# Kernel tuning notes

Hardware: AMD Instinct MI355X
Metric: run time of the kernel (lower is better)

The kernel has to match this reference:

```python
import jax, jax.numpy as jnp
import numpy as np

B, C, H, W = 8, 512, 32, 32
NUM_HEADS = 8
HEAD_DIM = C // NUM_HEADS
SCALE = 1.0 / float(np.sqrt(HEAD_DIM))


def setup_inputs() -> dict:
    key = jax.random.key(0)
    ks = jax.random.split(key, 6)
    x = jax.random.normal(ks[0], (B, C, H, W), dtype=jnp.float32)
    attn_mask = jax.random.randint(ks[1], (B, H, W), 0, 2).astype(jnp.bool_)
    # 1x1 conv weights are equivalent to channel matmuls: (out_ch, in_ch)
    w_std = 1.0 / float(np.sqrt(C))
    qkv_w = jax.random.uniform(ks[2], (3 * C, C), jnp.float32, -w_std, w_std)
    qkv_b = jax.random.uniform(ks[3], (3 * C,), jnp.float32, -w_std, w_std)
    proj_w = jax.random.uniform(ks[4], (C, C), jnp.float32, -w_std, w_std)
    proj_b = jax.random.uniform(ks[5], (C,), jnp.float32, -w_std, w_std)
    return {"x": x, "attn_mask": attn_mask, "qkv_w": qkv_w, "qkv_b": qkv_b,
            "proj_w": proj_w, "proj_b": proj_b}


def reference(x, attn_mask, qkv_w, qkv_b, proj_w, proj_b):
    b, c, h, w = x.shape
    S = h * w
    neg = jnp.finfo(x.dtype).min
    # qkv 1x1 conv: (B,3C,H,W)
    qkv = jnp.einsum('oc,bchw->bohw', qkv_w, x) + qkv_b[None, :, None, None]
    q, k, v = jnp.split(qkv, 3, axis=1)

    def split_heads(z):
        # (B, C, H, W) -> (B, heads, head_dim, S)
        return z.reshape(b, NUM_HEADS, HEAD_DIM, S)

    q, k, v = split_heads(q), split_heads(k), split_heads(v)
    # scores[s,t] = sum_d q[d,s] * k[d,t]
    scores = jnp.einsum('bhds,bhdt->bhst', q, k) * SCALE
    idx = jnp.arange(S)
    causal = (idx[None, :] > idx[:, None])[None, None]  # (1,1,S,S), True above diag
    scores = jnp.where(causal, neg, scores)
    kpm = attn_mask.reshape(b, 1, 1, S)  # key padding mask, True = mask out
    scores = jnp.where(kpm, neg, scores)
    attn = jax.nn.softmax(scores, axis=-1)
    # ctx[d,s] = sum_t v[d,t] * attn[s,t]
    ctx = jnp.einsum('bhdt,bhst->bhds', v, attn)
    ctx = ctx.reshape(b, c, h, w)
    out = jnp.einsum('oc,bchw->bohw', proj_w, ctx) + proj_b[None, :, None, None]
    return out
```

## Files before the change

### kernel.cpp

```cpp
#include <hip/hip_runtime.h>
#include <cfloat>
#include <math.h>

#define SB 1024
#define CC 512
#define NB 8
#define NH 8
#define HD 64

typedef short short8 __attribute__((ext_vector_type(8)));
typedef short s16x4 __attribute__((ext_vector_type(4)));
typedef float f32x4 __attribute__((ext_vector_type(4)));

__device__ __forceinline__ short f2bs(float f) {
    union { float f; unsigned u; } x; x.f = f;
    unsigned r = x.u + 0x7fffu + ((x.u >> 16) & 1u);
    return (short)(r >> 16);
}

__device__ __forceinline__ float bs2f(short s) {
    union { unsigned u; float f; } x;
    x.u = ((unsigned)(unsigned short)s) << 16;
    return x.f;
}

__device__ __forceinline__ void gload16(const void* g, void* l) {
    __builtin_amdgcn_global_load_lds(
        (const __attribute__((address_space(1))) unsigned int*)g,
        (__attribute__((address_space(3))) unsigned int*)l, 16, 0, 0);
}

__device__ __forceinline__ int sidx(int row, int colb) {
    return row * 64 + ((colb ^ ((row & 7) << 4)) >> 1);
}

__global__ __launch_bounds__(256)
void cvt_weights(const float* __restrict__ w1, const float* __restrict__ w2,
                 short* __restrict__ o1, short* __restrict__ o2)
{
    const int i4 = blockIdx.x * 256 + threadIdx.x;
    const int N1 = 1536 * 512 / 4;
    if (i4 < N1) {
        float4 v = *(const float4*)&w1[(size_t)i4 * 4];
        s16x4 p; p[0] = f2bs(v.x); p[1] = f2bs(v.y); p[2] = f2bs(v.z); p[3] = f2bs(v.w);
        *(s16x4*)&o1[(size_t)i4 * 4] = p;
    } else {
        const int j = i4 - N1;
        float4 v = *(const float4*)&w2[(size_t)j * 4];
        s16x4 p; p[0] = f2bs(v.x); p[1] = f2bs(v.y); p[2] = f2bs(v.z); p[3] = f2bs(v.w);
        *(s16x4*)&o2[(size_t)j * 4] = p;
    }
}

__global__ __launch_bounds__(256)
void transpose_x(const float* __restrict__ x, short* __restrict__ xT)
{
    const int bs = blockIdx.x, bc = blockIdx.y, b = blockIdx.z;
    const int tid = threadIdx.x;
    __shared__ short T[64][72];
    {
        const int cl = tid >> 4;
        const int s4 = (tid & 15) * 4;
        #pragma unroll
        for (int r = 0; r < 4; ++r) {
            const int c = cl + 16 * r;
            float4 v = *(const float4*)&x[((size_t)b * CC + bc * 64 + c) * SB + bs * 64 + s4];
            T[s4 + 0][c] = f2bs(v.x); T[s4 + 1][c] = f2bs(v.y);
            T[s4 + 2][c] = f2bs(v.z); T[s4 + 3][c] = f2bs(v.w);
        }
    }
    __syncthreads();
    {
        const int sl = tid >> 2;
        const int c16 = (tid & 3) * 16;
        short8 v0 = *(const short8*)&T[sl][c16];
        short8 v1 = *(const short8*)&T[sl][c16 + 8];
        short* dst = &xT[((size_t)b * SB + bs * 64 + sl) * CC + bc * 64 + c16];
        *(short8*)&dst[0] = v0;
        *(short8*)&dst[8] = v1;
    }
}

__global__ __launch_bounds__(256)
void vmean_kernel(const short* __restrict__ vN, const int* __restrict__ mask,
                  float* __restrict__ vmean, float* __restrict__ maskf)
{
    const int gi = blockIdx.x * 256 + threadIdx.x;
    if (gi < NB * SB) maskf[gi] = (mask[gi] != 0) ? -FLT_MAX : 0.f;

    const int row = blockIdx.x * 4 + (threadIdx.x >> 6);
    const int lane = threadIdx.x & 63;
    const short* p = vN + (size_t)row * SB + lane * 16;
    short8 a = *(const short8*)&p[0];
    short8 b8 = *(const short8*)&p[8];
    float s = 0.f;
    #pragma unroll
    for (int j = 0; j < 8; ++j) s += bs2f(a[j]) + bs2f(b8[j]);
    #pragma unroll
    for (int o = 1; o < 64; o <<= 1) s += __shfl_xor(s, o, 64);
    if (lane == 0) vmean[row] = s * (1.f / 1024.f);
}

template<int MODE>
__global__ __launch_bounds__(256)
void gemm_bf16(const short* __restrict__ A, const float* __restrict__ bias,
               const short* __restrict__ BT,
               short* __restrict__ qTo, short* __restrict__ kTo,
               short* __restrict__ vo, float* __restrict__ fo)
{
    const int stile = blockIdx.x * 128;
    const int bo    = blockIdx.y;
    const int b     = blockIdx.z;
    const int tid   = threadIdx.x;
    const int wave = tid >> 6, lane = tid & 63, lg = lane >> 4, ln = lane & 15;
    const int wm = wave >> 1, wn = wave & 1;

    __shared__ short Al[128 * 64];
    __shared__ short Bl[128 * 64];

    f32x4 acc[4][4];
    #pragma unroll
    for (int mt = 0; mt < 4; ++mt)
        #pragma unroll
        for (int nt = 0; nt < 4; ++nt) acc[mt][nt] = (f32x4){0.f, 0.f, 0.f, 0.f};

    const char* Ab = (const char*)(A + (size_t)bo * 128 * 512);
    const char* Bb = (const char*)(BT + ((size_t)b * SB + stile) * 512);

    for (int kc = 0; kc < 512; kc += 64) {
        __syncthreads();
        #pragma unroll
        for (int sw = 0; sw < 4; ++sw) {
            const int lin = tid * 16 + sw * 4096;
            const int row = lin >> 7;
            const int scol = (lin & 127) ^ ((row & 7) << 4);
            gload16(Ab + ((size_t)row * 512 + kc) * 2 + scol,
                    (char*)Al + (wave << 10) + (sw << 12));
            gload16(Bb + ((size_t)row * 512 + kc) * 2 + scol,
                    (char*)Bl + (wave << 10) + (sw << 12));
        }
        __syncthreads();
        #pragma unroll
        for (int kk = 0; kk < 2; ++kk) {
            const int colb = kk * 64 + lg * 16;
            short8 a[4], bb[4];
            #pragma unroll
            for (int mt = 0; mt < 4; ++mt)
                a[mt] = *(const short8*)&Al[sidx(wm * 64 + mt * 16 + ln, colb)];
            #pragma unroll
            for (int nt = 0; nt < 4; ++nt)
                bb[nt] = *(const short8*)&Bl[sidx(wn * 64 + nt * 16 + ln, colb)];
            #pragma unroll
            for (int mt = 0; mt < 4; ++mt)
                #pragma unroll
                for (int nt = 0; nt < 4; ++nt)
                    acc[mt][nt] = __builtin_amdgcn_mfma_f32_16x16x32_bf16(
                        a[mt], bb[nt], acc[mt][nt], 0, 0, 0);
        }
    }

    const int s_base = stile + wn * 64;
    if (MODE == 0) {
        if (bo < 8) {
            short* dst = (bo < 4) ? qTo : kTo;
            const int h = (bo & 3) * 2 + wm;
            const float sc = (bo < 4) ? 0.18033688011112042f : 1.0f;
            #pragma unroll
            for (int mt = 0; mt < 4; ++mt) {
                const int d0 = mt * 16 + 4 * lg;
                const int o0 = bo * 128 + wm * 64 + d0;
                const float b0 = bias[o0], b1 = bias[o0 + 1],
                            b2 = bias[o0 + 2], b3 = bias[o0 + 3];
                #pragma unroll
                for (int nt = 0; nt < 4; ++nt) {
                    const int s = s_base + nt * 16 + ln;
                    s16x4 pk;
                    pk[0] = f2bs((acc[mt][nt][0] + b0) * sc);
                    pk[1] = f2bs((acc[mt][nt][1] + b1) * sc);
                    pk[2] = f2bs((acc[mt][nt][2] + b2) * sc);
                    pk[3] = f2bs((acc[mt][nt][3] + b3) * sc);
                    *(s16x4*)&dst[(((size_t)b * NH + h) * SB + s) * HD + d0] = pk;
                }
            }
        } else {
            #pragma unroll
            for (int mt = 0; mt < 4; ++mt) {
                const int cv0 = (bo - 8) * 128 + wm * 64 + mt * 16 + 4 * lg;
                #pragma unroll
                for (int r = 0; r < 4; ++r) {
                    const float bv = bias[1024 + cv0 + r];
                    #pragma unroll
                    for (int nt = 0; nt < 4; ++nt) {
                        const int s = s_base + nt * 16 + ln;
                        vo[((size_t)b * CC + cv0 + r) * SB + s] = f2bs(acc[mt][nt][r] + bv);
                    }
                }
            }
        }
    } else {
        #pragma unroll
        for (int mt = 0; mt < 4; ++mt) {
            #pragma unroll
            for (int r = 0; r < 4; ++r) {
                const int o = bo * 128 + wm * 64 + mt * 16 + 4 * lg + r;
                const float bv = bias[o];
                #pragma unroll
                for (int nt = 0; nt < 4; ++nt) {
                    const int s = s_base + nt * 16 + ln;
                    fo[((size_t)b * CC + o) * SB + s] = acc[mt][nt][r] + bv;
                }
            }
        }
    }
}

__global__ __launch_bounds__(256, 4)
void attn_mfma(const short* __restrict__ qT, const short* __restrict__ kT,
               const short* __restrict__ vN, const float* __restrict__ maskf,
               const float* __restrict__ vmean, short* __restrict__ ctxT)
{
    const int L  = blockIdx.x;
    const int qb = 15 - (L >> 6);
    const int bh = L & 63;
    const int b  = bh >> 3, h = bh & 7;
    const int tid = threadIdx.x;
    const int wave = tid >> 6;
    const int lane = tid & 63;
    const int lg = lane >> 4;
    const int ln = lane & 15;

    __shared__ short Ks[2][64 * 64];
    __shared__ short Vs[2][64 * 64];
    __shared__ float mskL[2][64];
    __shared__ short Ps[4][16][72];

    const char*  kbh = (const char*)(kT + (((size_t)b * NH + h) * SB) * HD);
    const char*  vbh = (const char*)(vN + ((size_t)b * CC + h * HD) * SB);
    const float* mb  = maskf + (size_t)b * SB;

    short8 qa0, qa1;
    {
        const short* qrow = qT + (((size_t)b * NH + h) * SB + qb * 64 + wave * 16 + ln) * HD;
        qa0 = *(const short8*)&qrow[8 * lg];
        qa1 = *(const short8*)&qrow[32 + 8 * lg];
    }

    float m_ = -FLT_MAX, l_ = 0.f;
    f32x4 acc[4];
    #pragma unroll
    for (int nt = 0; nt < 4; ++nt) acc[nt] = (f32x4){0.f, 0.f, 0.f, 0.f};

    auto stage = [&](int tb, int bi) {
        #pragma unroll
        for (int sw = 0; sw < 2; ++sw) {
            const int lin = tid * 16 + sw * 4096;
            const int row = lin >> 7;
            const int scol = (lin & 127) ^ ((row & 7) << 4);
            gload16(kbh + (size_t)tb * 128 + row * 128 + scol,
                    (char*)&Ks[bi][0] + (wave << 10) + (sw << 12));
            gload16(vbh + (size_t)row * (SB * 2) + tb * 2 + scol,
                    (char*)&Vs[bi][0] + (wave << 10) + (sw << 12));
        }
        if (tid < 64) mskL[bi][tid] = mb[tb + tid];
    };

    int cur = 0;
    stage(0, 0);
    __syncthreads();

    for (int t = 0; t <= qb; ++t) {
        if (t < qb) stage((t + 1) * 64, cur ^ 1);

        f32x4 sc[4];
        #pragma unroll
        for (int nt = 0; nt < 4; ++nt) {
            short8 kb0 = *(const short8*)&Ks[cur][sidx(ln + 16 * nt, lg * 16)];
            short8 kb1 = *(const short8*)&Ks[cur][sidx(ln + 16 * nt, 64 + lg * 16)];
            f32x4 z = (f32x4){0.f, 0.f, 0.f, 0.f};
            z = __builtin_amdgcn_mfma_f32_16x16x32_bf16(kb0, qa0, z, 0, 0, 0);
            z = __builtin_amdgcn_mfma_f32_16x16x32_bf16(kb1, qa1, z, 0, 0, 0);
            sc[nt] = z;
        }

        #pragma unroll
        for (int nt = 0; nt < 4; ++nt) {
            const float4 mf = *(const float4*)&mskL[cur][16 * nt + 4 * lg];
            sc[nt][0] += mf.x; sc[nt][1] += mf.y;
            sc[nt][2] += mf.z; sc[nt][3] += mf.w;
        }
        if (t == qb) {
            const int so = wave * 16 + ln;
            #pragma unroll
            for (int nt = 0; nt < 4; ++nt)
                #pragma unroll
                for (int r = 0; r < 4; ++r)
                    if (16 * nt + 4 * lg + r > so) sc[nt][r] = -FLT_MAX;
        }

        float mx = sc[0][0];
        #pragma unroll
        for (int nt = 0; nt < 4; ++nt)
            #pragma unroll
            for (int r = 0; r < 4; ++r)
                if (nt | r) mx = fmaxf(mx, sc[nt][r]);
        mx = fmaxf(mx, __shfl_xor(mx, 16, 64));
        mx = fmaxf(mx, __shfl_xor(mx, 32, 64));

        if (!__all(mx <= m_ + 11.5f)) {
            const float mnew = fmaxf(m_, mx);
            const float fq = exp2f(m_ - mnew);
            l_ *= fq;
            #pragma unroll
            for (int nt = 0; nt < 4; ++nt)
                #pragma unroll
                for (int r = 0; r < 4; ++r) acc[nt][r] *= fq;
            m_ = mnew;
        }

        float rs = 0.f;
        #pragma unroll
        for (int nt = 0; nt < 4; ++nt) {
            s16x4 pk;
            #pragma unroll
            for (int r = 0; r < 4; ++r) {
                const float p = exp2f(sc[nt][r] - m_);
                rs += p;
                pk[r] = f2bs(p);
            }
            *(s16x4*)&Ps[wave][ln][16 * nt + 4 * lg] = pk;
        }
        rs += __shfl_xor(rs, 16, 64);
        rs += __shfl_xor(rs, 32, 64);
        l_ += rs;

        const short8 pa0 = *(const short8*)&Ps[wave][ln][8 * lg];
        const short8 pa1 = *(const short8*)&Ps[wave][ln][32 + 8 * lg];
        #pragma unroll
        for (int nt = 0; nt < 4; ++nt) {
            short8 va0 = *(const short8*)&Vs[cur][sidx(16 * nt + ln, lg * 16)];
            short8 va1 = *(const short8*)&Vs[cur][sidx(16 * nt + ln, 64 + lg * 16)];
            acc[nt] = __builtin_amdgcn_mfma_f32_16x16x32_bf16(va0, pa0, acc[nt], 0, 0, 0);
            acc[nt] = __builtin_amdgcn_mfma_f32_16x16x32_bf16(va1, pa1, acc[nt], 0, 0, 0);
        }

        if (t < qb) {
            __syncthreads();
            cur ^= 1;
        }
    }

    const float rl = 1.f / l_;
    const bool dead = (m_ == -FLT_MAX);
    const float* vmb = vmean + (size_t)b * CC + h * HD;
    const int s = qb * 64 + wave * 16 + ln;
    short* crow = ctxT + ((size_t)b * SB + s) * CC + h * HD;
    #pragma unroll
    for (int nt = 0; nt < 4; ++nt) {
        const int d0 = 16 * nt + 4 * lg;
        const float4 vm4 = *(const float4*)&vmb[d0];
        s16x4 pk;
        pk[0] = f2bs(dead ? vm4.x : acc[nt][0] * rl);
        pk[1] = f2bs(dead ? vm4.y : acc[nt][1] * rl);
        pk[2] = f2bs(dead ? vm4.z : acc[nt][2] * rl);
        pk[3] = f2bs(dead ? vm4.w : acc[nt][3] * rl);
        *(s16x4*)&crow[d0] = pk;
    }
}

extern "C" void kernel_launch(void* const* d_in, const int* in_sizes, int n_in,
                              void* d_out, int out_size, void* d_ws, size_t ws_size,
                              hipStream_t stream) {
    const float* x      = (const float*)d_in[0];
    const int*   amask  = (const int*)d_in[1];
    const float* qkv_w  = (const float*)d_in[2];
    const float* qkv_b  = (const float*)d_in[3];
    const float* proj_w = (const float*)d_in[4];
    const float* proj_b = (const float*)d_in[5];
    float* out = (float*)d_out;

    short* xT    = (short*)d_ws;
    short* w1b   = xT  + (size_t)NB * SB * CC;
    short* w2b   = w1b + (size_t)1536 * 512;
    short* qT    = w2b + (size_t)512 * 512;
    short* kT    = qT  + (size_t)NB * NH * SB * HD;
    short* vN    = kT  + (size_t)NB * NH * SB * HD;
    short* ctxT  = vN  + (size_t)NB * CC * SB;
    float* vmean = (float*)(ctxT + (size_t)NB * SB * CC);
    float* maskf = vmean + (size_t)NB * CC;

    cvt_weights<<<1024, 256, 0, stream>>>(qkv_w, proj_w, w1b, w2b);
    transpose_x<<<dim3(SB / 64, CC / 64, NB), 256, 0, stream>>>(x, xT);
    gemm_bf16<0><<<dim3(8, 12, NB), 256, 0, stream>>>(
        w1b, qkv_b, xT, qT, kT, vN, nullptr);
    vmean_kernel<<<NB * CC / 4, 256, 0, stream>>>(vN, amask, vmean, maskf);
    attn_mfma<<<dim3(1024, 1, 1), 256, 0, stream>>>(qT, kT, vN, maskf, vmean, ctxT);
    gemm_bf16<1><<<dim3(8, 4, NB), 256, 0, stream>>>(
        w2b, proj_b, ctxT, nullptr, nullptr, nullptr, out);
}
```

Baseline: 85.14 us.

## Merge prep kernels, fuse V-mean into QKV GEMM, pair query blocks in attention

The weight conversion, x transpose, mask conversion and vmean zeroing now run as one prep launch. The V row means are accumulated with atomics in the QKV GEMM epilogue, which removes the separate vmean kernel. The attention kernel now uses 512-thread blocks that each handle two query blocks (2p and 2p+1) and share the K/V tile loads between them. The two halves do unequal work, so waves of the lower query block sit idle on the last tile, and the atomics add contention and make the sums nondeterministic.

```diff
diff --git a/kernel.cpp b/kernel.cpp
--- a/kernel.cpp
+++ b/kernel.cpp
@@ -18,12 +18,6 @@
     return (short)(r >> 16);
 }
 
-__device__ __forceinline__ float bs2f(short s) {
-    union { unsigned u; float f; } x;
-    x.u = ((unsigned)(unsigned short)s) << 16;
-    return x.f;
-}
-
 __device__ __forceinline__ void gload16(const void* g, void* l) {
     __builtin_amdgcn_global_load_lds(
         (const __attribute__((address_space(1))) unsigned int*)g,
@@ -35,70 +29,59 @@
 }
 
 __global__ __launch_bounds__(256)
-void cvt_weights(const float* __restrict__ w1, const float* __restrict__ w2,
-                 short* __restrict__ o1, short* __restrict__ o2)
+void prep(const float* __restrict__ w1, const float* __restrict__ w2,
+          short* __restrict__ o1, short* __restrict__ o2,
+          const float* __restrict__ x, short* __restrict__ xT,
+          const int* __restrict__ mask, float* __restrict__ maskf,
+          float* __restrict__ vmean)
 {
-    const int i4 = blockIdx.x * 256 + threadIdx.x;
-    const int N1 = 1536 * 512 / 4;
-    if (i4 < N1) {
-        float4 v = *(const float4*)&w1[(size_t)i4 * 4];
-        s16x4 p; p[0] = f2bs(v.x); p[1] = f2bs(v.y); p[2] = f2bs(v.z); p[3] = f2bs(v.w);
-        *(s16x4*)&o1[(size_t)i4 * 4] = p;
+    const int B = blockIdx.x;
+    const int tid = threadIdx.x;
+    if (B < 1024) {
+        const int i4 = B * 256 + tid;
+        const int N1 = 1536 * 512 / 4;
+        if (i4 < N1) {
+            float4 v = *(const float4*)&w1[(size_t)i4 * 4];
+            s16x4 p; p[0] = f2bs(v.x); p[1] = f2bs(v.y); p[2] = f2bs(v.z); p[3] = f2bs(v.w);
+            *(s16x4*)&o1[(size_t)i4 * 4] = p;
+        } else {
+            const int j = i4 - N1;
+            float4 v = *(const float4*)&w2[(size_t)j * 4];
+            s16x4 p; p[0] = f2bs(v.x); p[1] = f2bs(v.y); p[2] = f2bs(v.z); p[3] = f2bs(v.w);
+            *(s16x4*)&o2[(size_t)j * 4] = p;
+        }
+    } else if (B < 2048) {
+        const int idx = B - 1024;
+        const int bs = idx & 15, bc = (idx >> 4) & 7, b = idx >> 7;
+        __shared__ short T[64][72];
+        {
+            const int cl = tid >> 4;
+            const int s4 = (tid & 15) * 4;
+            #pragma unroll
+            for (int r = 0; r < 4; ++r) {
+                const int c = cl + 16 * r;
+                float4 v = *(const float4*)&x[((size_t)b * CC + bc * 64 + c) * SB + bs * 64 + s4];
+                T[s4 + 0][c] = f2bs(v.x); T[s4 + 1][c] = f2bs(v.y);
+                T[s4 + 2][c] = f2bs(v.z); T[s4 + 3][c] = f2bs(v.w);
+            }
+        }
+        __syncthreads();
+        {
+            const int sl = tid >> 2;
+            const int c16 = (tid & 3) * 16;
+            short8 v0 = *(const short8*)&T[sl][c16];
+            short8 v1 = *(const short8*)&T[sl][c16 + 8];
+            short* dst = &xT[((size_t)b * SB + bs * 64 + sl) * CC + bc * 64 + c16];
+            *(short8*)&dst[0] = v0;
+            *(short8*)&dst[8] = v1;
+        }
+    } else if (B < 2080) {
+        const int gi = (B - 2048) * 256 + tid;
+        if (gi < NB * SB) maskf[gi] = (mask[gi] != 0) ? -FLT_MAX : 0.f;
     } else {
-        const int j = i4 - N1;
-        float4 v = *(const float4*)&w2[(size_t)j * 4];
-        s16x4 p; p[0] = f2bs(v.x); p[1] = f2bs(v.y); p[2] = f2bs(v.z); p[3] = f2bs(v.w);
-        *(s16x4*)&o2[(size_t)j * 4] = p;
-    }
-}
-
-__global__ __launch_bounds__(256)
-void transpose_x(const float* __restrict__ x, short* __restrict__ xT)
-{
-    const int bs = blockIdx.x, bc = blockIdx.y, b = blockIdx.z;
-    const int tid = threadIdx.x;
-    __shared__ short T[64][72];
-    {
-        const int cl = tid >> 4;
-        const int s4 = (tid & 15) * 4;
-        #pragma unroll
-        for (int r = 0; r < 4; ++r) {
-            const int c = cl + 16 * r;
-            float4 v = *(const float4*)&x[((size_t)b * CC + bc * 64 + c) * SB + bs * 64 + s4];
-            T[s4 + 0][c] = f2bs(v.x); T[s4 + 1][c] = f2bs(v.y);
-            T[s4 + 2][c] = f2bs(v.z); T[s4 + 3][c] = f2bs(v.w);
-        }
-    }
-    __syncthreads();
-    {
-        const int sl = tid >> 2;
-        const int c16 = (tid & 3) * 16;
-        short8 v0 = *(const short8*)&T[sl][c16];
-        short8 v1 = *(const short8*)&T[sl][c16 + 8];
-        short* dst = &xT[((size_t)b * SB + bs * 64 + sl) * CC + bc * 64 + c16];
-        *(short8*)&dst[0] = v0;
-        *(short8*)&dst[8] = v1;
-    }
-}
-
-__global__ __launch_bounds__(256)
-void vmean_kernel(const short* __restrict__ vN, const int* __restrict__ mask,
-                  float* __restrict__ vmean, float* __restrict__ maskf)
-{
-    const int gi = blockIdx.x * 256 + threadIdx.x;
-    if (gi < NB * SB) maskf[gi] = (mask[gi] != 0) ? -FLT_MAX : 0.f;
-
-    const int row = blockIdx.x * 4 + (threadIdx.x >> 6);
-    const int lane = threadIdx.x & 63;
-    const short* p = vN + (size_t)row * SB + lane * 16;
-    short8 a = *(const short8*)&p[0];
-    short8 b8 = *(const short8*)&p[8];
-    float s = 0.f;
-    #pragma unroll
-    for (int j = 0; j < 8; ++j) s += bs2f(a[j]) + bs2f(b8[j]);
-    #pragma unroll
-    for (int o = 1; o < 64; o <<= 1) s += __shfl_xor(s, o, 64);
-    if (lane == 0) vmean[row] = s * (1.f / 1024.f);
+        const int i = (B - 2080) * 256 + tid;
+        if (i < NB * CC) vmean[i] = 0.f;
+    }
 }
 
 template<int MODE>
@@ -106,7 +89,8 @@
 void gemm_bf16(const short* __restrict__ A, const float* __restrict__ bias,
                const short* __restrict__ BT,
                short* __restrict__ qTo, short* __restrict__ kTo,
-               short* __restrict__ vo, float* __restrict__ fo)
+               short* __restrict__ vo, float* __restrict__ fo,
+               float* __restrict__ vmean)
 {
     const int stile = blockIdx.x * 128;
     const int bo    = blockIdx.y;
@@ -189,11 +173,19 @@
                 #pragma unroll
                 for (int r = 0; r < 4; ++r) {
                     const float bv = bias[1024 + cv0 + r];
+                    float part = 0.f;
                     #pragma unroll
                     for (int nt = 0; nt < 4; ++nt) {
                         const int s = s_base + nt * 16 + ln;
-                        vo[((size_t)b * CC + cv0 + r) * SB + s] = f2bs(acc[mt][nt][r] + bv);
+                        const float val = acc[mt][nt][r] + bv;
+                        part += val;
+                        vo[((size_t)b * CC + cv0 + r) * SB + s] = f2bs(val);
                     }
+                    #pragma unroll
+                    for (int o = 1; o < 16; o <<= 1)
+                        part += __shfl_xor(part, o, 64);
+                    if (ln == 0)
+                        atomicAdd(&vmean[(size_t)b * CC + cv0 + r], part);
                 }
             }
         }
@@ -214,13 +206,13 @@
     }
 }
 
-__global__ __launch_bounds__(256, 4)
+__global__ __launch_bounds__(512, 4)
 void attn_mfma(const short* __restrict__ qT, const short* __restrict__ kT,
                const short* __restrict__ vN, const float* __restrict__ maskf,
                const float* __restrict__ vmean, short* __restrict__ ctxT)
 {
     const int L  = blockIdx.x;
-    const int qb = 15 - (L >> 6);
+    const int p  = 7 - (L >> 6);
     const int bh = L & 63;
     const int b  = bh >> 3, h = bh & 7;
     const int tid = threadIdx.x;
@@ -229,10 +221,14 @@
     const int lg = lane >> 4;
     const int ln = lane & 15;
 
+    const int qbm  = 2 * p + (wave >> 2);
+    const int wsub = wave & 3;
+    const int tend = 2 * p + 1;
+
     __shared__ short Ks[2][64 * 64];
     __shared__ short Vs[2][64 * 64];
     __shared__ float mskL[2][64];
-    __shared__ short Ps[4][16][72];
+    __shared__ short Ps[8][16][72];
 
     const char*  kbh = (const char*)(kT + (((size_t)b * NH + h) * SB) * HD);
     const char*  vbh = (const char*)(vN + ((size_t)b * CC + h * HD) * SB);
@@ -240,7 +236,7 @@
 
     short8 qa0, qa1;
     {
-        const short* qrow = qT + (((size_t)b * NH + h) * SB + qb * 64 + wave * 16 + ln) * HD;
+        const short* qrow = qT + (((size_t)b * NH + h) * SB + qbm * 64 + wsub * 16 + ln) * HD;
         qa0 = *(const short8*)&qrow[8 * lg];
         qa1 = *(const short8*)&qrow[32 + 8 * lg];
     }
@@ -251,16 +247,13 @@
     for (int nt = 0; nt < 4; ++nt) acc[nt] = (f32x4){0.f, 0.f, 0.f, 0.f};
 
     auto stage = [&](int tb, int bi) {
-        #pragma unroll
-        for (int sw = 0; sw < 2; ++sw) {
-            const int lin = tid * 16 + sw * 4096;
-            const int row = lin >> 7;
-            const int scol = (lin & 127) ^ ((row & 7) << 4);
-            gload16(kbh + (size_t)tb * 128 + row * 128 + scol,
-                    (char*)&Ks[bi][0] + (wave << 10) + (sw << 12));
-            gload16(vbh + (size_t)row * (SB * 2) + tb * 2 + scol,
-                    (char*)&Vs[bi][0] + (wave << 10) + (sw << 12));
-        }
+        const int lin = tid * 16;
+        const int row = lin >> 7;
+        const int scol = (lin & 127) ^ ((row & 7) << 4);
+        gload16(kbh + (size_t)tb * 128 + row * 128 + scol,
+                (char*)&Ks[bi][0] + (wave << 10));
+        gload16(vbh + (size_t)row * (SB * 2) + tb * 2 + scol,
+                (char*)&Vs[bi][0] + (wave << 10));
         if (tid < 64) mskL[bi][tid] = mb[tb + tid];
     };
 
@@ -268,82 +261,85 @@
     stage(0, 0);
     __syncthreads();
 
-    for (int t = 0; t <= qb; ++t) {
-        if (t < qb) stage((t + 1) * 64, cur ^ 1);
-
-        f32x4 sc[4];
-        #pragma unroll
-        for (int nt = 0; nt < 4; ++nt) {
-            short8 kb0 = *(const short8*)&Ks[cur][sidx(ln + 16 * nt, lg * 16)];
-            short8 kb1 = *(const short8*)&Ks[cur][sidx(ln + 16 * nt, 64 + lg * 16)];
-            f32x4 z = (f32x4){0.f, 0.f, 0.f, 0.f};
-            z = __builtin_amdgcn_mfma_f32_16x16x32_bf16(kb0, qa0, z, 0, 0, 0);
-            z = __builtin_amdgcn_mfma_f32_16x16x32_bf16(kb1, qa1, z, 0, 0, 0);
-            sc[nt] = z;
-        }
-
-        #pragma unroll
-        for (int nt = 0; nt < 4; ++nt) {
-            const float4 mf = *(const float4*)&mskL[cur][16 * nt + 4 * lg];
-            sc[nt][0] += mf.x; sc[nt][1] += mf.y;
-            sc[nt][2] += mf.z; sc[nt][3] += mf.w;
-        }
-        if (t == qb) {
-            const int so = wave * 16 + ln;
+    for (int t = 0; t <= tend; ++t) {
+        if (t < tend) stage((t + 1) * 64, cur ^ 1);
+        const bool mine = (t <= qbm);
+
+        if (mine) {
+            f32x4 sc[4];
+            #pragma unroll
+            for (int nt = 0; nt < 4; ++nt) {
+                short8 kb0 = *(const short8*)&Ks[cur][sidx(ln + 16 * nt, lg * 16)];
+                short8 kb1 = *(const short8*)&Ks[cur][sidx(ln + 16 * nt, 64 + lg * 16)];
+                f32x4 z = (f32x4){0.f, 0.f, 0.f, 0.f};
+                z = __builtin_amdgcn_mfma_f32_16x16x32_bf16(kb0, qa0, z, 0, 0, 0);
+                z = __builtin_amdgcn_mfma_f32_16x16x32_bf16(kb1, qa1, z, 0, 0, 0);
+                sc[nt] = z;
+            }
+
+            #pragma unroll
+            for (int nt = 0; nt < 4; ++nt) {
+                const float4 mf = *(const float4*)&mskL[cur][16 * nt + 4 * lg];
+                sc[nt][0] += mf.x; sc[nt][1] += mf.y;
+                sc[nt][2] += mf.z; sc[nt][3] += mf.w;
+            }
+            if (t == qbm) {
+                const int so = wsub * 16 + ln;
+                #pragma unroll
+                for (int nt = 0; nt < 4; ++nt)
+                    #pragma unroll
+                    for (int r = 0; r < 4; ++r)
+                        if (16 * nt + 4 * lg + r > so) sc[nt][r] = -FLT_MAX;
+            }
+
+            float mx = sc[0][0];
             #pragma unroll
             for (int nt = 0; nt < 4; ++nt)
                 #pragma unroll
                 for (int r = 0; r < 4; ++r)
-                    if (16 * nt + 4 * lg + r > so) sc[nt][r] = -FLT_MAX;
-        }
-
-        float mx = sc[0][0];
-        #pragma unroll
-        for (int nt = 0; nt < 4; ++nt)
-            #pragma unroll
-            for (int r = 0; r < 4; ++r)
-                if (nt | r) mx = fmaxf(mx, sc[nt][r]);
-        mx = fmaxf(mx, __shfl_xor(mx, 16, 64));
-        mx = fmaxf(mx, __shfl_xor(mx, 32, 64));
-
-        if (!__all(mx <= m_ + 11.5f)) {
-            const float mnew = fmaxf(m_, mx);
-            const float fq = exp2f(m_ - mnew);
-            l_ *= fq;
-            #pragma unroll
-            for (int nt = 0; nt < 4; ++nt)
-                #pragma unroll
-                for (int r = 0; r < 4; ++r) acc[nt][r] *= fq;
-            m_ = mnew;
-        }
-
-        float rs = 0.f;
-        #pragma unroll
-        for (int nt = 0; nt < 4; ++nt) {
-            s16x4 pk;
-            #pragma unroll
-            for (int r = 0; r < 4; ++r) {
-                const float p = exp2f(sc[nt][r] - m_);
-                rs += p;
-                pk[r] = f2bs(p);
-            }
-            *(s16x4*)&Ps[wave][ln][16 * nt + 4 * lg] = pk;
-        }
-        rs += __shfl_xor(rs, 16, 64);
-        rs += __shfl_xor(rs, 32, 64);
-        l_ += rs;
-
-        const short8 pa0 = *(const short8*)&Ps[wave][ln][8 * lg];
-        const short8 pa1 = *(const short8*)&Ps[wave][ln][32 + 8 * lg];
-        #pragma unroll
-        for (int nt = 0; nt < 4; ++nt) {
-            short8 va0 = *(const short8*)&Vs[cur][sidx(16 * nt + ln, lg * 16)];
-            short8 va1 = *(const short8*)&Vs[cur][sidx(16 * nt + ln, 64 + lg * 16)];
-            acc[nt] = __builtin_amdgcn_mfma_f32_16x16x32_bf16(va0, pa0, acc[nt], 0, 0, 0);
-            acc[nt] = __builtin_amdgcn_mfma_f32_16x16x32_bf16(va1, pa1, acc[nt], 0, 0, 0);
-        }
-
-        if (t < qb) {
+                    if (nt | r) mx = fmaxf(mx, sc[nt][r]);
+            mx = fmaxf(mx, __shfl_xor(mx, 16, 64));
+            mx = fmaxf(mx, __shfl_xor(mx, 32, 64));
+
+            if (!__all(mx <= m_ + 11.5f)) {
+                const float mnew = fmaxf(m_, mx);
+                const float fq = exp2f(m_ - mnew);
+                l_ *= fq;
+                #pragma unroll
+                for (int nt = 0; nt < 4; ++nt)
+                    #pragma unroll
+                    for (int r = 0; r < 4; ++r) acc[nt][r] *= fq;
+                m_ = mnew;
+            }
+
+            float rs = 0.f;
+            #pragma unroll
+            for (int nt = 0; nt < 4; ++nt) {
+                s16x4 pk;
+                #pragma unroll
+                for (int r = 0; r < 4; ++r) {
+                    const float pv = exp2f(sc[nt][r] - m_);
+                    rs += pv;
+                    pk[r] = f2bs(pv);
+                }
+                *(s16x4*)&Ps[wave][ln][16 * nt + 4 * lg] = pk;
+            }
+            rs += __shfl_xor(rs, 16, 64);
+            rs += __shfl_xor(rs, 32, 64);
+            l_ += rs;
+
+            const short8 pa0 = *(const short8*)&Ps[wave][ln][8 * lg];
+            const short8 pa1 = *(const short8*)&Ps[wave][ln][32 + 8 * lg];
+            #pragma unroll
+            for (int nt = 0; nt < 4; ++nt) {
+                short8 va0 = *(const short8*)&Vs[cur][sidx(16 * nt + ln, lg * 16)];
+                short8 va1 = *(const short8*)&Vs[cur][sidx(16 * nt + ln, 64 + lg * 16)];
+                acc[nt] = __builtin_amdgcn_mfma_f32_16x16x32_bf16(va0, pa0, acc[nt], 0, 0, 0);
+                acc[nt] = __builtin_amdgcn_mfma_f32_16x16x32_bf16(va1, pa1, acc[nt], 0, 0, 0);
+            }
+        }
+
+        if (t < tend) {
             __syncthreads();
             cur ^= 1;
         }
@@ -352,17 +348,17 @@
     const float rl = 1.f / l_;
     const bool dead = (m_ == -FLT_MAX);
     const float* vmb = vmean + (size_t)b * CC + h * HD;
-    const int s = qb * 64 + wave * 16 + ln;
+    const int s = qbm * 64 + wsub * 16 + ln;
     short* crow = ctxT + ((size_t)b * SB + s) * CC + h * HD;
     #pragma unroll
     for (int nt = 0; nt < 4; ++nt) {
         const int d0 = 16 * nt + 4 * lg;
         const float4 vm4 = *(const float4*)&vmb[d0];
         s16x4 pk;
-        pk[0] = f2bs(dead ? vm4.x : acc[nt][0] * rl);
-        pk[1] = f2bs(dead ? vm4.y : acc[nt][1] * rl);
-        pk[2] = f2bs(dead ? vm4.z : acc[nt][2] * rl);
-        pk[3] = f2bs(dead ? vm4.w : acc[nt][3] * rl);
+        pk[0] = f2bs(dead ? vm4.x * (1.f / 1024.f) : acc[nt][0] * rl);
+        pk[1] = f2bs(dead ? vm4.y * (1.f / 1024.f) : acc[nt][1] * rl);
+        pk[2] = f2bs(dead ? vm4.z * (1.f / 1024.f) : acc[nt][2] * rl);
+        pk[3] = f2bs(dead ? vm4.w * (1.f / 1024.f) : acc[nt][3] * rl);
         *(s16x4*)&crow[d0] = pk;
     }
 }
@@ -388,12 +384,11 @@
     float* vmean = (float*)(ctxT + (size_t)NB * SB * CC);
     float* maskf = vmean + (size_t)NB * CC;
 
-    cvt_weights<<<1024, 256, 0, stream>>>(qkv_w, proj_w, w1b, w2b);
-    transpose_x<<<dim3(SB / 64, CC / 64, NB), 256, 0, stream>>>(x, xT);
+    prep<<<2096, 256, 0, stream>>>(qkv_w, proj_w, w1b, w2b, x, xT,
+                                   amask, maskf, vmean);
     gemm_bf16<0><<<dim3(8, 12, NB), 256, 0, stream>>>(
-        w1b, qkv_b, xT, qT, kT, vN, nullptr);
-    vmean_kernel<<<NB * CC / 4, 256, 0, stream>>>(vN, amask, vmean, maskf);
-    attn_mfma<<<dim3(1024, 1, 1), 256, 0, stream>>>(qT, kT, vN, maskf, vmean, ctxT);
+        w1b, qkv_b, xT, qT, kT, vN, nullptr, vmean);
+    attn_mfma<<<dim3(512, 1, 1), 512, 0, stream>>>(qT, kT, vN, maskf, vmean, ctxT);
     gemm_bf16<1><<<dim3(8, 4, NB), 256, 0, stream>>>(
-        w2b, proj_b, ctxT, nullptr, nullptr, nullptr, out);
-}
+        w2b, proj_b, ctxT, nullptr, nullptr, nullptr, out, nullptr);
+}
```

Result: slower. 89.11 us (+4.7%).
